# Kernel tuning notes

Hardware: AMD Instinct MI355X
Metric: run time of the kernel (lower is better)

Reference implementation:

```python
import jax, jax.numpy as jnp
import numpy as np

NEG_SLOPE = 0.2
EPS = 1e-16


def gat_layer(x, src, dst, W, a_src, a_dst, b, num_nodes, heads, out_ch):
    # x: [N, F_in], W: [F_in, heads*out_ch], a_src/a_dst: [heads, out_ch], b: [heads*out_ch]
    h = (x @ W).reshape(num_nodes, heads, out_ch)          # [N, H, C]
    e_src = jnp.einsum('nhc,hc->nh', h, a_src)             # [N, H]
    e_dst = jnp.einsum('nhc,hc->nh', h, a_dst)             # [N, H]
    e = jax.nn.leaky_relu(e_src[src] + e_dst[dst], NEG_SLOPE)  # [E, H]
    # segment softmax over incoming edges of each destination node
    m = jax.ops.segment_max(e, dst, num_segments=num_nodes)
    m = jnp.where(jnp.isfinite(m), m, 0.0)                 # empty segments -> 0
    p = jnp.exp(e - m[dst])
    s = jax.ops.segment_sum(p, dst, num_segments=num_nodes)
    alpha = p / (s[dst] + EPS)                             # [E, H]
    msg = h[src] * alpha[:, :, None]                       # [E, H, C]
    out = jax.ops.segment_sum(msg, dst, num_segments=num_nodes)  # [N, H, C]
    return out.reshape(num_nodes, heads * out_ch) + b


def setup_inputs() -> dict:
    key = jax.random.key(0)
    ks = jax.random.split(key, 10)
    N, E = 50000, 800000
    F_IN, H1, C1, NCLS = 128, 8, 8, 40
    x = jax.random.normal(ks[0], (N, F_IN), jnp.float32)
    edge_index = jax.random.randint(ks[1], (2, E), 0, N, dtype=jnp.int64)
    g = lambda k, shape, fan_in: jax.random.normal(k, shape, jnp.float32) / np.sqrt(fan_in)
    W1 = g(ks[2], (F_IN, H1 * C1), F_IN)
    a_src1 = g(ks[3], (H1, C1), C1)
    a_dst1 = g(ks[4], (H1, C1), C1)
    b1 = jnp.zeros((H1 * C1,), jnp.float32)
    W2 = g(ks[5], (H1 * C1, NCLS), H1 * C1)
    a_src2 = g(ks[6], (1, NCLS), NCLS)
    a_dst2 = g(ks[7], (1, NCLS), NCLS)
    b2 = jnp.zeros((NCLS,), jnp.float32)
    return dict(x=x, edge_index=edge_index, W1=W1, a_src1=a_src1, a_dst1=a_dst1, b1=b1,
                W2=W2, a_src2=a_src2, a_dst2=a_dst2, b2=b2)


def reference(x, edge_index, W1, a_src1, a_dst1, b1, W2, a_src2, a_dst2, b2):
    N = x.shape[0]
    src, dst = edge_index[0], edge_index[1]
    h = gat_layer(x, src, dst, W1, a_src1, a_dst1, b1, N, heads=8, out_ch=8)
    h = jax.nn.relu(h)
    out = gat_layer(h, src, dst, W2, a_src2, a_dst2, b2, N, heads=1, out_ch=40)
    return jax.nn.log_softmax(out, axis=-1)
```

## Files before the change

kernel.cpp:

```cpp
#include <hip/hip_runtime.h>
#include <math.h>

#define NEG_SLOPE 0.2f
#define GAT_EPS 1e-16f

__device__ __forceinline__ float lrelu(float v) {
    return v > 0.f ? v : NEG_SLOPE * v;
}

__global__ __launch_bounds__(256) void gemm1_kernel(
    const float* __restrict__ x, const float* __restrict__ W1,
    const float* __restrict__ a_src1, const float* __restrict__ a_dst1,
    float* __restrict__ h1, float* __restrict__ es1, float* __restrict__ ed1,
    int N)
{
    __shared__ float Ws[128 * 64];
    __shared__ float xs[4][128];

    int t = threadIdx.x;
    for (int i = t; i < 128 * 64; i += 256) Ws[i] = W1[i];

    int w    = t >> 6;
    int lane = t & 63;
    int n    = blockIdx.x * 4 + w;

    if (n < N) {
        xs[w][lane]      = x[(size_t)n * 128 + lane];
        xs[w][lane + 64] = x[(size_t)n * 128 + lane + 64];
    }
    __syncthreads();

    if (n < N) {
        float acc = 0.f;
        #pragma unroll
        for (int k = 0; k < 128; ++k)
            acc = fmaf(xs[w][k], Ws[k * 64 + lane], acc);
        h1[(size_t)n * 64 + lane] = acc;

        float ps = acc * a_src1[lane];
        float pd = acc * a_dst1[lane];
        #pragma unroll
        for (int m = 1; m < 8; m <<= 1) {
            ps += __shfl_xor(ps, m, 64);
            pd += __shfl_xor(pd, m, 64);
        }
        if ((lane & 7) == 0) {
            es1[(size_t)n * 8 + (lane >> 3)] = ps;
            ed1[(size_t)n * 8 + (lane >> 3)] = pd;
        }
    }
}

__global__ __launch_bounds__(256) void rank_kernel(
    const int* __restrict__ ei, int E,
    int* __restrict__ count, int* __restrict__ rank)
{
    int e = blockIdx.x * 256 + threadIdx.x;
    if (e >= E) return;
    rank[e] = atomicAdd(&count[ei[E + e]], 1);
}

__global__ __launch_bounds__(256) void scan1_kernel(
    const int* __restrict__ count, int* __restrict__ excl,
    int* __restrict__ btotal, int N)
{
    __shared__ int tmp[256];
    int t = threadIdx.x;
    int i = blockIdx.x * 256 + t;
    int v = (i < N) ? count[i] : 0;
    tmp[t] = v;
    __syncthreads();
    #pragma unroll
    for (int off = 1; off < 256; off <<= 1) {
        int add = (t >= off) ? tmp[t - off] : 0;
        __syncthreads();
        tmp[t] += add;
        __syncthreads();
    }
    if (i < N) excl[i] = tmp[t] - v;
    if (t == 255) btotal[blockIdx.x] = tmp[255];
}

__global__ __launch_bounds__(256) void scan2_kernel(int* __restrict__ btotal, int nb)
{
    __shared__ int tmp[256];
    int t = threadIdx.x;
    int v = (t < nb) ? btotal[t] : 0;
    tmp[t] = v;
    __syncthreads();
    #pragma unroll
    for (int off = 1; off < 256; off <<= 1) {
        int add = (t >= off) ? tmp[t - off] : 0;
        __syncthreads();
        tmp[t] += add;
        __syncthreads();
    }
    if (t < nb) btotal[t] = tmp[t] - v;
}

__global__ __launch_bounds__(256) void scan3_kernel(
    const int* __restrict__ excl, const int* __restrict__ btotal,
    int* __restrict__ row_start, int N, int E)
{
    int i = blockIdx.x * 256 + threadIdx.x;
    if (i < N) row_start[i] = excl[i] + btotal[blockIdx.x];
    if (i == 0) row_start[N] = E;
}

__global__ __launch_bounds__(256) void scatter_kernel(
    const int* __restrict__ ei, int E, const int* __restrict__ row_start,
    const int* __restrict__ rank, int* __restrict__ sorted_src)
{
    int e = blockIdx.x * 256 + threadIdx.x;
    if (e >= E) return;
    int d = ei[E + e];
    sorted_src[row_start[d] + rank[e]] = ei[e];
}

__global__ __launch_bounds__(256) void agg1_kernel(
    const int* __restrict__ row_start, const int* __restrict__ sorted_src,
    const float* __restrict__ h1, const float* __restrict__ es1,
    const float* __restrict__ ed1, const float* __restrict__ b1,
    const float* __restrict__ W2, const float* __restrict__ a_src2,
    const float* __restrict__ a_dst2,
    float* __restrict__ g, float* __restrict__ es2, float* __restrict__ ed2,
    int N)
{
    __shared__ float W2s[64 * 40];
    __shared__ float h2s[4][64];

    int t = threadIdx.x;
    for (int i = t; i < 64 * 40; i += 256) W2s[i] = W2[i];

    int w    = t >> 6;
    int lane = t & 63;
    int n    = blockIdx.x * 4 + w;
    int h    = lane >> 3;

    if (n < N) {
        int lo = row_start[n], hi = row_start[n + 1];
        float edh = ed1[(size_t)n * 8 + h];
        float acc = 0.f, den = 0.f;
        int e = lo;
        for (; e + 4 <= hi; e += 4) {
            int s0 = sorted_src[e],     s1 = sorted_src[e + 1];
            int s2 = sorted_src[e + 2], s3 = sorted_src[e + 3];
            float q0 = es1[(size_t)s0 * 8 + h], q1 = es1[(size_t)s1 * 8 + h];
            float q2 = es1[(size_t)s2 * 8 + h], q3 = es1[(size_t)s3 * 8 + h];
            float v0 = h1[(size_t)s0 * 64 + lane], v1 = h1[(size_t)s1 * 64 + lane];
            float v2 = h1[(size_t)s2 * 64 + lane], v3 = h1[(size_t)s3 * 64 + lane];
            float p0 = __expf(lrelu(q0 + edh)), p1 = __expf(lrelu(q1 + edh));
            float p2 = __expf(lrelu(q2 + edh)), p3 = __expf(lrelu(q3 + edh));
            acc = fmaf(v0, p0, acc); den += p0;
            acc = fmaf(v1, p1, acc); den += p1;
            acc = fmaf(v2, p2, acc); den += p2;
            acc = fmaf(v3, p3, acc); den += p3;
        }
        for (; e < hi; ++e) {
            int s = sorted_src[e];
            float p = __expf(lrelu(es1[(size_t)s * 8 + h] + edh));
            acc = fmaf(h1[(size_t)s * 64 + lane], p, acc);
            den += p;
        }
        float v = acc / (den + GAT_EPS) + b1[lane];
        h2s[w][lane] = v > 0.f ? v : 0.f;
    }
    __syncthreads();

    if (n < N) {
        float gv = 0.f;
        if (lane < 40) {
            #pragma unroll
            for (int k = 0; k < 64; ++k)
                gv = fmaf(h2s[w][k], W2s[k * 40 + lane], gv);
            g[(size_t)n * 40 + lane] = gv;
        }
        float ps = (lane < 40) ? gv * a_src2[lane] : 0.f;
        float pd = (lane < 40) ? gv * a_dst2[lane] : 0.f;
        #pragma unroll
        for (int m = 1; m < 64; m <<= 1) {
            ps += __shfl_xor(ps, m, 64);
            pd += __shfl_xor(pd, m, 64);
        }
        if (lane == 0) { es2[n] = ps; ed2[n] = pd; }
    }
}

__global__ __launch_bounds__(256) void agg2_kernel(
    const int* __restrict__ row_start, const int* __restrict__ sorted_src,
    const float* __restrict__ g, const float* __restrict__ es2,
    const float* __restrict__ ed2, const float* __restrict__ b2,
    float* __restrict__ out, int N)
{
    int t = threadIdx.x;
    int w = t >> 6, lane = t & 63;
    int n = blockIdx.x * 4 + w;
    if (n >= N) return;

    int lo = row_start[n], hi = row_start[n + 1];
    float dn = ed2[n];
    float acc = 0.f, den = 0.f;
    int e = lo;
    for (; e + 4 <= hi; e += 4) {
        int s0 = sorted_src[e],     s1 = sorted_src[e + 1];
        int s2 = sorted_src[e + 2], s3 = sorted_src[e + 3];
        float q0 = es2[s0], q1 = es2[s1], q2 = es2[s2], q3 = es2[s3];
        float v0 = 0.f, v1 = 0.f, v2 = 0.f, v3 = 0.f;
        if (lane < 40) {
            v0 = g[(size_t)s0 * 40 + lane];
            v1 = g[(size_t)s1 * 40 + lane];
            v2 = g[(size_t)s2 * 40 + lane];
            v3 = g[(size_t)s3 * 40 + lane];
        }
        float p0 = __expf(lrelu(q0 + dn)), p1 = __expf(lrelu(q1 + dn));
        float p2 = __expf(lrelu(q2 + dn)), p3 = __expf(lrelu(q3 + dn));
        acc = fmaf(v0, p0, acc); den += p0;
        acc = fmaf(v1, p1, acc); den += p1;
        acc = fmaf(v2, p2, acc); den += p2;
        acc = fmaf(v3, p3, acc); den += p3;
    }
    for (; e < hi; ++e) {
        int s = sorted_src[e];
        float p = __expf(lrelu(es2[s] + dn));
        den += p;
        if (lane < 40) acc = fmaf(g[(size_t)s * 40 + lane], p, acc);
    }

    float val = 0.f, v = -INFINITY;
    if (lane < 40) {
        val = acc / (den + GAT_EPS) + b2[lane];
        v = val;
    }
    float mx = v;
    #pragma unroll
    for (int m = 1; m < 64; m <<= 1)
        mx = fmaxf(mx, __shfl_xor(mx, m, 64));
    float ex = (lane < 40) ? __expf(val - mx) : 0.f;
    #pragma unroll
    for (int m = 1; m < 64; m <<= 1)
        ex += __shfl_xor(ex, m, 64);
    if (lane < 40)
        out[(size_t)n * 40 + lane] = val - mx - logf(ex);
}

extern "C" void kernel_launch(void* const* d_in, const int* in_sizes, int n_in,
                              void* d_out, int out_size, void* d_ws, size_t ws_size,
                              hipStream_t stream)
{
    const float* x      = (const float*)d_in[0];
    const int*   ei     = (const int*)d_in[1];
    const float* W1     = (const float*)d_in[2];
    const float* a_src1 = (const float*)d_in[3];
    const float* a_dst1 = (const float*)d_in[4];
    const float* b1     = (const float*)d_in[5];
    const float* W2     = (const float*)d_in[6];
    const float* a_src2 = (const float*)d_in[7];
    const float* a_dst2 = (const float*)d_in[8];
    const float* b2     = (const float*)d_in[9];
    float* out = (float*)d_out;

    int N = in_sizes[0] / 128;
    int E = in_sizes[1] / 2;
    int nb  = (N + 255) / 256;
    int nb4 = (N + 3) / 4;
    int eb  = (E + 255) / 256;

    float* ws = (float*)d_ws;
    size_t off = 0;
    float* h1  = ws + off; off += (size_t)N * 64;
    float* es1 = ws + off; off += (size_t)N * 8;
    float* ed1 = ws + off; off += (size_t)N * 8;
    float* g   = ws + off; off += (size_t)N * 40;
    float* es2 = ws + off; off += (size_t)N;
    float* ed2 = ws + off; off += (size_t)N;
    int* row_start  = (int*)(ws + off); off += (size_t)N + 1;
    int* sorted_src = (int*)(ws + off); off += (size_t)E;
    int* rank       = (int*)(ws + off); off += (size_t)E;
    int* excl       = (int*)(ws + off); off += (size_t)N;
    int* btotal     = (int*)(ws + off); off += 256;
    int* count      = (int*)(ws + off); off += (size_t)N;

    hipMemsetAsync(count, 0, (size_t)N * sizeof(int), stream);

    rank_kernel<<<eb, 256, 0, stream>>>(ei, E, count, rank);
    scan1_kernel<<<nb, 256, 0, stream>>>(count, excl, btotal, N);
    scan2_kernel<<<1, 256, 0, stream>>>(btotal, nb);
    scan3_kernel<<<nb, 256, 0, stream>>>(excl, btotal, row_start, N, E);
    scatter_kernel<<<eb, 256, 0, stream>>>(ei, E, row_start, rank, sorted_src);
    gemm1_kernel<<<nb4, 256, 0, stream>>>(x, W1, a_src1, a_dst1, h1, es1, ed1, N);
    agg1_kernel<<<nb4, 256, 0, stream>>>(row_start, sorted_src, h1, es1, ed1,
                                         b1, W2, a_src2, a_dst2, g, es2, ed2, N);
    agg2_kernel<<<nb4, 256, 0, stream>>>(row_start, sorted_src, g, es2, ed2,
                                         b2, out, N);
}
```

Before: 307.3 us.

## Store gathered features in bf16, fuse rank with GEMM, single-block scan

Intermediate node features h1 and g are stored as bf16, halving the bytes moved by the random-access gathers in both aggregation kernels. The edge-ranking atomics and the first-layer GEMM now run in one launch as disjoint block ranges. The three-kernel prefix scan is replaced by a single 1024-thread block that does a chunked serial-plus-parallel scan. Together these cut gather bandwidth and launch count, at the cost of bf16 rounding error in the features and a serial, strided scan inside one block.

```diff
diff --git a/kernel.cpp b/kernel.cpp
--- a/kernel.cpp
+++ b/kernel.cpp
@@ -1,4 +1,5 @@
 #include <hip/hip_runtime.h>
+#include <hip/hip_bf16.h>
 #include <math.h>
 
 #define NEG_SLOPE 0.2f
@@ -8,21 +9,30 @@
     return v > 0.f ? v : NEG_SLOPE * v;
 }
 
-__global__ __launch_bounds__(256) void gemm1_kernel(
+__global__ __launch_bounds__(256) void prep_kernel(
+    const int* __restrict__ ei, int E,
+    int* __restrict__ count, int* __restrict__ rank,
     const float* __restrict__ x, const float* __restrict__ W1,
     const float* __restrict__ a_src1, const float* __restrict__ a_dst1,
-    float* __restrict__ h1, float* __restrict__ es1, float* __restrict__ ed1,
-    int N)
-{
+    __hip_bfloat16* __restrict__ h1, float* __restrict__ es1,
+    float* __restrict__ ed1, int N, int eb)
+{
+    if ((int)blockIdx.x < eb) {
+        int e = blockIdx.x * 256 + threadIdx.x;
+        if (e < E) rank[e] = atomicAdd(&count[ei[E + e]], 1);
+        return;
+    }
+
     __shared__ float Ws[128 * 64];
     __shared__ float xs[4][128];
 
+    int b = blockIdx.x - eb;
     int t = threadIdx.x;
     for (int i = t; i < 128 * 64; i += 256) Ws[i] = W1[i];
 
     int w    = t >> 6;
     int lane = t & 63;
-    int n    = blockIdx.x * 4 + w;
+    int n    = b * 4 + w;
 
     if (n < N) {
         xs[w][lane]      = x[(size_t)n * 128 + lane];
@@ -35,7 +45,7 @@
         #pragma unroll
         for (int k = 0; k < 128; ++k)
             acc = fmaf(xs[w][k], Ws[k * 64 + lane], acc);
-        h1[(size_t)n * 64 + lane] = acc;
+        h1[(size_t)n * 64 + lane] = __float2bfloat16(acc);
 
         float ps = acc * a_src1[lane];
         float pd = acc * a_dst1[lane];
@@ -51,60 +61,32 @@
     }
 }
 
-__global__ __launch_bounds__(256) void rank_kernel(
-    const int* __restrict__ ei, int E,
-    int* __restrict__ count, int* __restrict__ rank)
-{
-    int e = blockIdx.x * 256 + threadIdx.x;
-    if (e >= E) return;
-    rank[e] = atomicAdd(&count[ei[E + e]], 1);
-}
-
-__global__ __launch_bounds__(256) void scan1_kernel(
-    const int* __restrict__ count, int* __restrict__ excl,
-    int* __restrict__ btotal, int N)
-{
-    __shared__ int tmp[256];
-    int t = threadIdx.x;
-    int i = blockIdx.x * 256 + t;
-    int v = (i < N) ? count[i] : 0;
-    tmp[t] = v;
+__global__ __launch_bounds__(1024) void scanall_kernel(
+    const int* __restrict__ count, int* __restrict__ row_start, int N, int E)
+{
+    __shared__ int part[1024];
+    int t = threadIdx.x;
+    int chunk = (N + 1023) / 1024;
+    int lo = t * chunk; if (lo > N) lo = N;
+    int hi = lo + chunk; if (hi > N) hi = N;
+
+    int sum = 0;
+    for (int i = lo; i < hi; ++i) sum += count[i];
+    part[t] = sum;
     __syncthreads();
     #pragma unroll
-    for (int off = 1; off < 256; off <<= 1) {
-        int add = (t >= off) ? tmp[t - off] : 0;
+    for (int off = 1; off < 1024; off <<= 1) {
+        int add = (t >= off) ? part[t - off] : 0;
         __syncthreads();
-        tmp[t] += add;
+        part[t] += add;
         __syncthreads();
     }
-    if (i < N) excl[i] = tmp[t] - v;
-    if (t == 255) btotal[blockIdx.x] = tmp[255];
-}
-
-__global__ __launch_bounds__(256) void scan2_kernel(int* __restrict__ btotal, int nb)
-{
-    __shared__ int tmp[256];
-    int t = threadIdx.x;
-    int v = (t < nb) ? btotal[t] : 0;
-    tmp[t] = v;
-    __syncthreads();
-    #pragma unroll
-    for (int off = 1; off < 256; off <<= 1) {
-        int add = (t >= off) ? tmp[t - off] : 0;
-        __syncthreads();
-        tmp[t] += add;
-        __syncthreads();
-    }
-    if (t < nb) btotal[t] = tmp[t] - v;
-}
-
-__global__ __launch_bounds__(256) void scan3_kernel(
-    const int* __restrict__ excl, const int* __restrict__ btotal,
-    int* __restrict__ row_start, int N, int E)
-{
-    int i = blockIdx.x * 256 + threadIdx.x;
-    if (i < N) row_start[i] = excl[i] + btotal[blockIdx.x];
-    if (i == 0) row_start[N] = E;
+    int run = part[t] - sum;
+    for (int i = lo; i < hi; ++i) {
+        row_start[i] = run;
+        run += count[i];
+    }
+    if (t == 0) row_start[N] = E;
 }
 
 __global__ __launch_bounds__(256) void scatter_kernel(
@@ -119,12 +101,12 @@
 
 __global__ __launch_bounds__(256) void agg1_kernel(
     const int* __restrict__ row_start, const int* __restrict__ sorted_src,
-    const float* __restrict__ h1, const float* __restrict__ es1,
+    const __hip_bfloat16* __restrict__ h1, const float* __restrict__ es1,
     const float* __restrict__ ed1, const float* __restrict__ b1,
     const float* __restrict__ W2, const float* __restrict__ a_src2,
     const float* __restrict__ a_dst2,
-    float* __restrict__ g, float* __restrict__ es2, float* __restrict__ ed2,
-    int N)
+    __hip_bfloat16* __restrict__ g, float* __restrict__ es2,
+    float* __restrict__ ed2, int N)
 {
     __shared__ float W2s[64 * 40];
     __shared__ float h2s[4][64];
@@ -147,8 +129,10 @@
             int s2 = sorted_src[e + 2], s3 = sorted_src[e + 3];
             float q0 = es1[(size_t)s0 * 8 + h], q1 = es1[(size_t)s1 * 8 + h];
             float q2 = es1[(size_t)s2 * 8 + h], q3 = es1[(size_t)s3 * 8 + h];
-            float v0 = h1[(size_t)s0 * 64 + lane], v1 = h1[(size_t)s1 * 64 + lane];
-            float v2 = h1[(size_t)s2 * 64 + lane], v3 = h1[(size_t)s3 * 64 + lane];
+            float v0 = __bfloat162float(h1[(size_t)s0 * 64 + lane]);
+            float v1 = __bfloat162float(h1[(size_t)s1 * 64 + lane]);
+            float v2 = __bfloat162float(h1[(size_t)s2 * 64 + lane]);
+            float v3 = __bfloat162float(h1[(size_t)s3 * 64 + lane]);
             float p0 = __expf(lrelu(q0 + edh)), p1 = __expf(lrelu(q1 + edh));
             float p2 = __expf(lrelu(q2 + edh)), p3 = __expf(lrelu(q3 + edh));
             acc = fmaf(v0, p0, acc); den += p0;
@@ -159,7 +143,7 @@
         for (; e < hi; ++e) {
             int s = sorted_src[e];
             float p = __expf(lrelu(es1[(size_t)s * 8 + h] + edh));
-            acc = fmaf(h1[(size_t)s * 64 + lane], p, acc);
+            acc = fmaf(__bfloat162float(h1[(size_t)s * 64 + lane]), p, acc);
             den += p;
         }
         float v = acc / (den + GAT_EPS) + b1[lane];
@@ -173,7 +157,7 @@
             #pragma unroll
             for (int k = 0; k < 64; ++k)
                 gv = fmaf(h2s[w][k], W2s[k * 40 + lane], gv);
-            g[(size_t)n * 40 + lane] = gv;
+            g[(size_t)n * 40 + lane] = __float2bfloat16(gv);
         }
         float ps = (lane < 40) ? gv * a_src2[lane] : 0.f;
         float pd = (lane < 40) ? gv * a_dst2[lane] : 0.f;
@@ -188,7 +172,7 @@
 
 __global__ __launch_bounds__(256) void agg2_kernel(
     const int* __restrict__ row_start, const int* __restrict__ sorted_src,
-    const float* __restrict__ g, const float* __restrict__ es2,
+    const __hip_bfloat16* __restrict__ g, const float* __restrict__ es2,
     const float* __restrict__ ed2, const float* __restrict__ b2,
     float* __restrict__ out, int N)
 {
@@ -207,10 +191,10 @@
         float q0 = es2[s0], q1 = es2[s1], q2 = es2[s2], q3 = es2[s3];
         float v0 = 0.f, v1 = 0.f, v2 = 0.f, v3 = 0.f;
         if (lane < 40) {
-            v0 = g[(size_t)s0 * 40 + lane];
-            v1 = g[(size_t)s1 * 40 + lane];
-            v2 = g[(size_t)s2 * 40 + lane];
-            v3 = g[(size_t)s3 * 40 + lane];
+            v0 = __bfloat162float(g[(size_t)s0 * 40 + lane]);
+            v1 = __bfloat162float(g[(size_t)s1 * 40 + lane]);
+            v2 = __bfloat162float(g[(size_t)s2 * 40 + lane]);
+            v3 = __bfloat162float(g[(size_t)s3 * 40 + lane]);
         }
         float p0 = __expf(lrelu(q0 + dn)), p1 = __expf(lrelu(q1 + dn));
         float p2 = __expf(lrelu(q2 + dn)), p3 = __expf(lrelu(q3 + dn));
@@ -223,7 +207,8 @@
         int s = sorted_src[e];
         float p = __expf(lrelu(es2[s] + dn));
         den += p;
-        if (lane < 40) acc = fmaf(g[(size_t)s * 40 + lane], p, acc);
+        if (lane < 40)
+            acc = fmaf(__bfloat162float(g[(size_t)s * 40 + lane]), p, acc);
     }
 
     float val = 0.f, v = -INFINITY;
@@ -261,33 +246,29 @@
 
     int N = in_sizes[0] / 128;
     int E = in_sizes[1] / 2;
-    int nb  = (N + 255) / 256;
     int nb4 = (N + 3) / 4;
     int eb  = (E + 255) / 256;
 
     float* ws = (float*)d_ws;
     size_t off = 0;
-    float* h1  = ws + off; off += (size_t)N * 64;
+    __hip_bfloat16* h1 = (__hip_bfloat16*)(ws + off); off += (size_t)N * 32;
     float* es1 = ws + off; off += (size_t)N * 8;
     float* ed1 = ws + off; off += (size_t)N * 8;
-    float* g   = ws + off; off += (size_t)N * 40;
+    __hip_bfloat16* g  = (__hip_bfloat16*)(ws + off); off += (size_t)N * 20;
     float* es2 = ws + off; off += (size_t)N;
     float* ed2 = ws + off; off += (size_t)N;
     int* row_start  = (int*)(ws + off); off += (size_t)N + 1;
     int* sorted_src = (int*)(ws + off); off += (size_t)E;
     int* rank       = (int*)(ws + off); off += (size_t)E;
-    int* excl       = (int*)(ws + off); off += (size_t)N;
-    int* btotal     = (int*)(ws + off); off += 256;
     int* count      = (int*)(ws + off); off += (size_t)N;
 
     hipMemsetAsync(count, 0, (size_t)N * sizeof(int), stream);
 
-    rank_kernel<<<eb, 256, 0, stream>>>(ei, E, count, rank);
-    scan1_kernel<<<nb, 256, 0, stream>>>(count, excl, btotal, N);
-    scan2_kernel<<<1, 256, 0, stream>>>(btotal, nb);
-    scan3_kernel<<<nb, 256, 0, stream>>>(excl, btotal, row_start, N, E);
+    prep_kernel<<<eb + nb4, 256, 0, stream>>>(ei, E, count, rank,
+                                              x, W1, a_src1, a_dst1,
+                                              h1, es1, ed1, N, eb);
+    scanall_kernel<<<1, 1024, 0, stream>>>(count, row_start, N, E);
     scatter_kernel<<<eb, 256, 0, stream>>>(ei, E, row_start, rank, sorted_src);
-    gemm1_kernel<<<nb4, 256, 0, stream>>>(x, W1, a_src1, a_dst1, h1, es1, ed1, N);
     agg1_kernel<<<nb4, 256, 0, stream>>>(row_start, sorted_src, h1, es1, ed1,
                                          b1, W2, a_src2, a_dst2, g, es2, ed2, N);
     agg2_kernel<<<nb4, 256, 0, stream>>>(row_start, sorted_src, g, es2, ed2,
```

Result: slower. 366.3 us (+19.2%).
